# Optimization experiments

Hardware: AMD Instinct MI355X
Metric: run time of the kernel (lower is better)

Reference implementation:

```python
import jax, jax.numpy as jnp
import numpy as np
from jax import lax

D_MODEL = 1024
D_STATE = 16
D_CONV = 4
EXPAND = 2
D_INNER = EXPAND * D_MODEL          # 2048
DT_RANK = (D_MODEL + 15) // 16      # 64


def setup_inputs() -> dict:
    key = jax.random.key(0)
    ks = jax.random.split(key, 12)
    B, L = 2, 2048
    s = lambda *sh: 1.0 / np.sqrt(sh[-1])
    inp = {
        "x": jax.random.normal(ks[0], (B, L, D_MODEL), jnp.float32),
        "in_proj_w": jax.random.normal(ks[1], (2 * D_INNER, D_MODEL), jnp.float32) * s(0, D_MODEL),
        "conv_w": jax.random.normal(ks[2], (D_INNER, 1, D_CONV), jnp.float32) * s(0, D_CONV),
        "conv_b": jax.random.normal(ks[3], (D_INNER,), jnp.float32) * 0.01,
        "x_proj_w": jax.random.normal(ks[4], (DT_RANK + 2 * D_STATE, D_INNER), jnp.float32) * s(0, D_INNER),
        "dt_proj_w": jax.random.normal(ks[5], (D_INNER, DT_RANK), jnp.float32) * s(0, DT_RANK),
        "dt_proj_b": jax.random.normal(ks[6], (D_INNER,), jnp.float32) * 0.1 - 4.0,  # softplus(dt) small
        "A_log": jnp.log(jnp.broadcast_to(jnp.arange(1, D_STATE + 1, dtype=jnp.float32), (D_INNER, D_STATE))),
        "D": jnp.ones((D_INNER,), jnp.float32),
        "out_proj_w": jax.random.normal(ks[7], (D_MODEL, D_INNER), jnp.float32) * s(0, D_INNER),
        "ln_w": jnp.ones((D_MODEL,), jnp.float32),
        "ln_b": jnp.zeros((D_MODEL,), jnp.float32),
    }
    return inp


def _mamba(x, in_proj_w, conv_w, conv_b, x_proj_w, dt_proj_w, dt_proj_b, A_log, D, out_proj_w):
    B, L, _ = x.shape
    xz = jnp.einsum("bld,ed->ble", x, in_proj_w)          # [B,L,2*d_inner]
    xi, z = jnp.split(xz, 2, axis=-1)                       # each [B,L,d_inner]

    # causal depthwise conv1d over time
    xt = jnp.transpose(xi, (0, 2, 1))                       # [B,d_inner,L]
    xc = lax.conv_general_dilated(
        xt, conv_w, window_strides=(1,), padding=[(D_CONV - 1, 0)],
        dimension_numbers=("NCH", "OIH", "NCH"), feature_group_count=D_INNER)
    xc = jax.nn.silu(xc + conv_b[None, :, None])            # [B,d_inner,L]
    u = jnp.transpose(xc, (0, 2, 1))                        # [B,L,d_inner]

    x_dbl = jnp.einsum("bld,ed->ble", u, x_proj_w)          # [B,L,dt_rank+2N]
    dt, Bm, Cm = jnp.split(x_dbl, [DT_RANK, DT_RANK + D_STATE], axis=-1)
    delta = jax.nn.softplus(jnp.einsum("blr,dr->bld", dt, dt_proj_w) + dt_proj_b)  # [B,L,d_inner]

    A = -jnp.exp(A_log)                                     # [d_inner,N]

    def step(h, inputs):
        d_t, B_t, C_t, u_t = inputs                         # [B,d], [B,N], [B,N], [B,d]
        dA = jnp.exp(d_t[..., None] * A)                    # [B,d_inner,N]
        h = dA * h + (d_t * u_t)[..., None] * B_t[:, None, :]
        y_t = jnp.einsum("bdn,bn->bd", h, C_t)
        return h, y_t

    xs = (jnp.transpose(delta, (1, 0, 2)), jnp.transpose(Bm, (1, 0, 2)),
          jnp.transpose(Cm, (1, 0, 2)), jnp.transpose(u, (1, 0, 2)))
    h0 = jnp.zeros((B, D_INNER, D_STATE), x.dtype)
    _, ys = lax.scan(step, h0, xs)                          # ys [L,B,d_inner]
    y = jnp.transpose(ys, (1, 0, 2)) + u * D                # skip connection
    y = y * jax.nn.silu(z)                                  # gate
    return jnp.einsum("bld,ed->ble", y, out_proj_w)         # [B,L,d_model]


def reference(x, in_proj_w, conv_w, conv_b, x_proj_w, dt_proj_w, dt_proj_b,
              A_log, D, out_proj_w, ln_w, ln_b):
    residual = x
    y = _mamba(x, in_proj_w, conv_w, conv_b, x_proj_w, dt_proj_w, dt_proj_b,
               A_log, D, out_proj_w)
    # dropout is identity in eval; residual + LayerNorm
    h = y + residual
    mu = jnp.mean(h, axis=-1, keepdims=True)
    var = jnp.var(h, axis=-1, keepdims=True)
    return (h - mu) * lax.rsqrt(var + 1e-5) * ln_w + ln_b
```

## Files before the change

### kernel.cpp

```cpp
#include <hip/hip_runtime.h>

typedef unsigned short u16;
typedef __attribute__((ext_vector_type(8))) short bf8_t;
typedef __attribute__((ext_vector_type(4))) float f4_t;
typedef __attribute__((ext_vector_type(4))) unsigned short u16x4;
typedef __attribute__((ext_vector_type(8))) unsigned short u16x8;

__device__ __forceinline__ float b2f(u16 h) {
  union { unsigned u; float f; } v; v.u = ((unsigned)h) << 16; return v.f;
}
__device__ __forceinline__ u16 f2b(float f) {
  union { float f; unsigned u; } v; v.f = f;
  unsigned u = v.u;
  u += 0x7fffu + ((u >> 16) & 1u);
  return (u16)(u >> 16);
}

#define AS1C(p) ((const __attribute__((address_space(1))) void*)(p))
#define AS3(p)  ((__attribute__((address_space(3))) void*)(p))

__global__ __launch_bounds__(256)
void cvt_all(const float* __restrict__ x, const float* __restrict__ inW,
             const float* __restrict__ xprojW, const float* __restrict__ dtW,
             const float* __restrict__ outW,
             u16* __restrict__ xb, u16* __restrict__ inWb, u16* __restrict__ xpb,
             u16* __restrict__ dtWb, u16* __restrict__ outWb)
{
  int i = blockIdx.x * 256 + threadIdx.x;
  if (i >= 2703360) return;
  const float* s; u16* d; int off;
  if (i < 1048576)      { s = x;      d = xb;    off = i; }
  else if (i < 2097152) { s = inW;    d = inWb;  off = i - 1048576; }
  else if (i < 2146304) { s = xprojW; d = xpb;   off = i - 2097152; }
  else if (i < 2179072) { s = dtW;    d = dtWb;  off = i - 2146304; }
  else                  { s = outW;   d = outWb; off = i - 2179072; }
  f4_t v = *(const f4_t*)(s + (size_t)off * 4);
  u16x4 o;
#pragma unroll
  for (int j = 0; j < 4; ++j) o[j] = f2b(v[j]);
  *(u16x4*)(d + (size_t)off * 4) = o;
}

__device__ __forceinline__ void stage64(const u16* g, int ld, int row0, int rowmax,
                                        int k0, u16* lds, int wid, int lane) {
  int qg = (lane & 7) ^ ((lane >> 3) & 7);
#pragma unroll
  for (int c = 0; c < 4; ++c) {
    int chunk = wid * 4 + c;
    int r = row0 + chunk * 8 + (lane >> 3);
    if (r > rowmax) r = rowmax;
    const u16* gp = g + (size_t)r * ld + k0 + qg * 8;
    __builtin_amdgcn_global_load_lds(AS1C(gp), AS3(lds + chunk * 512), 16, 0, 0);
  }
}

template<int EPI>
__device__ __forceinline__ void gemm_body(const u16* __restrict__ A, int lda,
             const u16* __restrict__ Bt, int ldb,
             int Kblk, int Nact,
             u16* __restrict__ o16, float* __restrict__ of32,
             float* __restrict__ of32b, const float* __restrict__ biasf)
{
  __shared__ u16 lsA[128 * 64];
  __shared__ u16 lsB[128 * 64];
  const int tid = threadIdx.x;
  const int wid = tid >> 6, lane = tid & 63;
  const int wm = wid >> 1, wn = wid & 1;
  const int lrow = lane & 15;
  const int kq = lane >> 4;
  const int sw = lrow & 7;
  const int m0 = blockIdx.y * 128;
  const int n0 = (EPI == 1) ? 0 : blockIdx.x * 128;
  int kbase = 0;
  if (EPI == 1) kbase = blockIdx.x * Kblk;

  f4_t acc[4][4];
#pragma unroll
  for (int i = 0; i < 4; ++i)
#pragma unroll
    for (int j = 0; j < 4; ++j) acc[i][j] = {0.f, 0.f, 0.f, 0.f};

  for (int kt = kbase; kt < kbase + Kblk; kt += 64) {
    stage64(A,  lda, m0, 0x3fffffff, kt, lsA, wid, lane);
    stage64(Bt, ldb, n0, Nact - 1,   kt, lsB, wid, lane);
    __syncthreads();
#pragma unroll
    for (int h = 0; h < 2; ++h) {
      const int lk = ((h * 4 + kq) ^ sw) * 8;
      bf8_t af[4], bfr[4];
#pragma unroll
      for (int mi = 0; mi < 4; ++mi)
        af[mi] = *(const bf8_t*)&lsA[(wm * 64 + mi * 16 + lrow) * 64 + lk];
#pragma unroll
      for (int ni = 0; ni < 4; ++ni)
        bfr[ni] = *(const bf8_t*)&lsB[(wn * 64 + ni * 16 + lrow) * 64 + lk];
#pragma unroll
      for (int mi = 0; mi < 4; ++mi)
#pragma unroll
        for (int ni = 0; ni < 4; ++ni)
          acc[mi][ni] = __builtin_amdgcn_mfma_f32_16x16x32_bf16(af[mi], bfr[ni], acc[mi][ni], 0, 0, 0);
    }
    __syncthreads();
  }

  const int rq = (lane >> 4) * 4;
#pragma unroll
  for (int mi = 0; mi < 4; ++mi) {
#pragma unroll
    for (int ni = 0; ni < 4; ++ni) {
#pragma unroll
      for (int r = 0; r < 4; ++r) {
        int m = m0 + wm * 64 + mi * 16 + rq + r;
        int n = n0 + wn * 64 + ni * 16 + lrow;
        float v = acc[mi][ni][r];
        if (EPI == 1) {
          if (n < 96) of32[((size_t)blockIdx.x * 4096 + m) * 96 + n] = v;
        } else if (EPI == 2) {
          float t = v + biasf[n];
          float sp = (t > 20.f) ? t : log1pf(__expf(t));
          o16[(size_t)m * 2048 + n] = f2b(sp);
        }
      }
    }
  }
}

__global__ __launch_bounds__(256)
void gemm_xp(const u16* A, int lda, const u16* Bt, int ldb, int Kblk, int Nact,
             u16* o16, float* of32, float* of32b, const float* biasf)
{ gemm_body<1>(A, lda, Bt, ldb, Kblk, Nact, o16, of32, of32b, biasf); }

__global__ __launch_bounds__(256)
void gemm_dt(const u16* A, int lda, const u16* Bt, int ldb, int Kblk, int Nact,
             u16* o16, float* of32, float* of32b, const float* biasf)
{ gemm_body<2>(A, lda, Bt, ldb, Kblk, Nact, o16, of32, of32b, biasf); }


__device__ __forceinline__ void stageu(const u16* __restrict__ g, int ld,
                                       int row0, int k0, u16* ldsu,
                                       int wid, int lane) {
  int qg = (lane & 7) ^ ((lane >> 3) & 7);
#pragma unroll
  for (int j = 0; j < 2; ++j) {
    int rr = j * 64 + wid * 8 + (lane >> 3);
    const u16* gp = g + (size_t)(row0 + rr) * ld + k0 + qg * 8;
    __builtin_amdgcn_global_load_lds(AS1C(gp), AS3(ldsu + (j * 512 + wid * 64) * 8), 16, 0, 0);
  }
}

#define G8_BAR()   __builtin_amdgcn_s_barrier()
#define G8_LGKM0() do { asm volatile("s_waitcnt lgkmcnt(0)" ::: "memory"); \
                        __builtin_amdgcn_sched_barrier(0); } while (0)
#define G8_VM(N)   do { asm volatile("s_waitcnt vmcnt(" #N ")" ::: "memory"); \
                        __builtin_amdgcn_sched_barrier(0); } while (0)

#define RD_A(base, MH) do { \
  _Pragma("unroll") \
  for (int mi_ = 0; mi_ < 4; ++mi_) { \
    af[mi_][0] = *(const bf8_t*)((base) + arow + ((MH) * 64 + mi_ * 16) * 64 + aq0); \
    af[mi_][1] = *(const bf8_t*)((base) + arow + ((MH) * 64 + mi_ * 16) * 64 + aq1); \
  } } while (0)

#define RD_B(base, NH) do { \
  _Pragma("unroll") \
  for (int ni_ = 0; ni_ < 2; ++ni_) { \
    bfr[NH][ni_][0] = *(const bf8_t*)((base) + brow + ((NH) * 32 + ni_ * 16) * 64 + aq0); \
    bfr[NH][ni_][1] = *(const bf8_t*)((base) + brow + ((NH) * 32 + ni_ * 16) * 64 + aq1); \
  } } while (0)

#define MMA(MH, NH) do { \
  __builtin_amdgcn_s_setprio(1); \
  _Pragma("unroll") \
  for (int mi_ = 0; mi_ < 4; ++mi_) \
    _Pragma("unroll") \
    for (int ni_ = 0; ni_ < 2; ++ni_) { \
      acc[(MH) * 4 + mi_][(NH) * 2 + ni_] = __builtin_amdgcn_mfma_f32_16x16x32_bf16( \
          af[mi_][0], bfr[NH][ni_][0], acc[(MH) * 4 + mi_][(NH) * 2 + ni_], 0, 0, 0); \
      acc[(MH) * 4 + mi_][(NH) * 2 + ni_] = __builtin_amdgcn_mfma_f32_16x16x32_bf16( \
          af[mi_][1], bfr[NH][ni_][1], acc[(MH) * 4 + mi_][(NH) * 2 + ni_], 0, 0, 0); \
    } \
  __builtin_amdgcn_s_setprio(0); \
} while (0)

__global__ __launch_bounds__(512, 2)
void gemm8_in(const u16* __restrict__ A, const u16* __restrict__ Bt,
              u16* __restrict__ o16)
{
  __shared__ u16 ls[65536];
  const int tid = threadIdx.x;
  const int wid = tid >> 6, lane = tid & 63;
  const int wm = wid >> 2, wn = wid & 3;
  const int lrow = lane & 15;
  const int kq = lane >> 4;
  const int sw = lrow & 7;
  const int m0 = blockIdx.y * 256;
  const int n0 = blockIdx.x * 256;
  u16* lsA0 = ls;
  u16* lsB0 = ls + 16384;
  u16* lsA1 = ls + 32768;
  u16* lsB1 = ls + 49152;
  const int arow = (wm * 128 + lrow) * 64;
  const int brow = (wn * 64 + lrow) * 64;
  const int aq0 = (kq ^ sw) * 8;
  const int aq1 = ((4 + kq) ^ sw) * 8;

  f4_t acc[8][4];
#pragma unroll
  for (int i = 0; i < 8; ++i)
#pragma unroll
    for (int j = 0; j < 4; ++j) acc[i][j] = {0.f, 0.f, 0.f, 0.f};
  bf8_t af[4][2];
  bf8_t bfr[2][2][2];

  stageu(A,  1024, m0,        0, lsA0,        wid, lane);
  stageu(A,  1024, m0 + 128,  0, lsA0 + 8192, wid, lane);
  stageu(Bt, 1024, n0,        0, lsB0,        wid, lane);
  stageu(Bt, 1024, n0 + 128,  0, lsB0 + 8192, wid, lane);
  stageu(Bt, 1024, n0,       64, lsB1,        wid, lane);
  stageu(Bt, 1024, n0 + 128, 64, lsB1 + 8192, wid, lane);
  G8_VM(4); G8_BAR();

#pragma unroll 1
  for (int i = 0; i < 7; ++i) {
    const int ka1 = (2 * i + 1) * 64;
    const int k2  = ka1 + 64;
    const int kb3 = ka1 + 128;
    RD_A(lsA0, 0); RD_B(lsB0, 0); RD_B(lsB0, 1);
    stageu(A, 1024, m0,       ka1, lsA1,        wid, lane);
    stageu(A, 1024, m0 + 128, ka1, lsA1 + 8192, wid, lane);
    G8_BAR(); G8_LGKM0(); MMA(0, 0); MMA(0, 1); G8_BAR();
    RD_A(lsA0, 1);
    stageu(Bt, 1024, n0,       k2, lsB0,        wid, lane);
    stageu(Bt, 1024, n0 + 128, k2, lsB0 + 8192, wid, lane);
    G8_BAR(); G8_LGKM0(); MMA(1, 0); MMA(1, 1); G8_VM(4); G8_BAR();
    RD_A(lsA1, 0); RD_B(lsB1, 0); RD_B(lsB1, 1);
    stageu(A, 1024, m0,       k2, lsA0,        wid, lane);
    stageu(A, 1024, m0 + 128, k2, lsA0 + 8192, wid, lane);
    G8_BAR(); G8_LGKM0(); MMA(0, 0); MMA(0, 1); G8_BAR();
    RD_A(lsA1, 1);
    stageu(Bt, 1024, n0,       kb3, lsB1,        wid, lane);
    stageu(Bt, 1024, n0 + 128, kb3, lsB1 + 8192, wid, lane);
    G8_BAR(); G8_LGKM0(); MMA(1, 0); MMA(1, 1); G8_VM(4); G8_BAR();
  }

  {
    const int ka1 = 960;
    RD_A(lsA0, 0); RD_B(lsB0, 0); RD_B(lsB0, 1);
    stageu(A, 1024, m0,       ka1, lsA1,        wid, lane);
    stageu(A, 1024, m0 + 128, ka1, lsA1 + 8192, wid, lane);
    G8_BAR(); G8_LGKM0(); MMA(0, 0); MMA(0, 1); G8_BAR();
    RD_A(lsA0, 1);
    G8_BAR(); G8_LGKM0(); MMA(1, 0); MMA(1, 1); G8_VM(0); G8_BAR();
    RD_A(lsA1, 0); RD_B(lsB1, 0); RD_B(lsB1, 1);
    G8_BAR(); G8_LGKM0(); MMA(0, 0); MMA(0, 1); G8_BAR();
    RD_A(lsA1, 1);
    G8_LGKM0(); MMA(1, 0); MMA(1, 1);
  }

  const int rq = (lane >> 4) * 4;
#pragma unroll
  for (int mi = 0; mi < 8; ++mi) {
#pragma unroll
    for (int ni = 0; ni < 4; ++ni) {
#pragma unroll
      for (int r = 0; r < 4; ++r) {
        int m = m0 + wm * 128 + mi * 16 + rq + r;
        int n = n0 + wn * 64 + ni * 16 + lrow;
        float v = acc[mi][ni][r];
        if (n < 2048) o16[(size_t)m * 2048 + n] = f2b(v);
        else          o16[(size_t)8388608 + (size_t)m * 2048 + (n - 2048)] = f2b(v);
      }
    }
  }
}


#define ORD_A(base, MH) do { \
  _Pragma("unroll") \
  for (int mi_ = 0; mi_ < 2; ++mi_) { \
    af[mi_][0] = *(const bf8_t*)((base) + arow + ((MH) * 32 + mi_ * 16) * 64 + aq0); \
    af[mi_][1] = *(const bf8_t*)((base) + arow + ((MH) * 32 + mi_ * 16) * 64 + aq1); \
  } } while (0)

#define OMMA(MH, NH) do { \
  __builtin_amdgcn_s_setprio(1); \
  _Pragma("unroll") \
  for (int mi_ = 0; mi_ < 2; ++mi_) \
    _Pragma("unroll") \
    for (int ni_ = 0; ni_ < 2; ++ni_) { \
      acc[(MH) * 2 + mi_][(NH) * 2 + ni_] = __builtin_amdgcn_mfma_f32_16x16x32_bf16( \
          af[mi_][0], bfr[NH][ni_][0], acc[(MH) * 2 + mi_][(NH) * 2 + ni_], 0, 0, 0); \
      acc[(MH) * 2 + mi_][(NH) * 2 + ni_] = __builtin_amdgcn_mfma_f32_16x16x32_bf16( \
          af[mi_][1], bfr[NH][ni_][1], acc[(MH) * 2 + mi_][(NH) * 2 + ni_], 0, 0, 0); \
    } \
  __builtin_amdgcn_s_setprio(0); \
} while (0)

__global__ __launch_bounds__(512, 2)
void gemm8_out(const u16* __restrict__ A, const u16* __restrict__ Bt,
               float* __restrict__ of32, float* __restrict__ of32b)
{
  __shared__ u16 ls[49152];
  const int tid = threadIdx.x;
  const int wid = tid >> 6, lane = tid & 63;
  const int wm = wid >> 2, wn = wid & 3;
  const int lrow = lane & 15;
  const int kq = lane >> 4;
  const int sw = lrow & 7;
  const int m0 = blockIdx.y * 128;
  const int n0 = blockIdx.x * 256;
  const int kbase = blockIdx.z * 1024;
  u16* lsA0 = ls;
  u16* lsB0 = ls + 8192;
  u16* lsA1 = ls + 24576;
  u16* lsB1 = ls + 32768;
  const int arow = (wm * 64 + lrow) * 64;
  const int brow = (wn >> 1) * 8192 + ((wn & 1) * 64 + lrow) * 64;
  const int aq0 = (kq ^ sw) * 8;
  const int aq1 = ((4 + kq) ^ sw) * 8;

  f4_t acc[4][4];
#pragma unroll
  for (int i = 0; i < 4; ++i)
#pragma unroll
    for (int j = 0; j < 4; ++j) acc[i][j] = {0.f, 0.f, 0.f, 0.f};
  bf8_t af[2][2];
  bf8_t bfr[2][2][2];

  stageu(A,  2048, m0,        kbase,      lsA0,        wid, lane);
  stageu(Bt, 2048, n0,        kbase,      lsB0,        wid, lane);
  stageu(Bt, 2048, n0 + 128,  kbase,      lsB0 + 8192, wid, lane);
  stageu(Bt, 2048, n0,        kbase + 64, lsB1,        wid, lane);
  stageu(Bt, 2048, n0 + 128,  kbase + 64, lsB1 + 8192, wid, lane);
  G8_VM(4); G8_BAR();

#pragma unroll 1
  for (int i = 0; i < 7; ++i) {
    const int k1 = kbase + (2 * i + 1) * 64, k2 = k1 + 64, k3 = k1 + 128;
    ORD_A(lsA0, 0); RD_B(lsB0, 0);
    stageu(A, 2048, m0, k1, lsA1, wid, lane);
    G8_BAR(); G8_LGKM0(); OMMA(0, 0); G8_BAR();
    RD_B(lsB0, 1);
    G8_BAR(); G8_LGKM0(); OMMA(0, 1); G8_BAR();
    ORD_A(lsA0, 1);
    stageu(Bt, 2048, n0, k2, lsB0, wid, lane);
    G8_BAR(); G8_LGKM0(); OMMA(1, 0); G8_BAR();
    stageu(Bt, 2048, n0 + 128, k2, lsB0 + 8192, wid, lane);
    G8_BAR(); G8_LGKM0(); OMMA(1, 1); G8_VM(4); G8_BAR();
    ORD_A(lsA1, 0); RD_B(lsB1, 0);
    stageu(A, 2048, m0, k2, lsA0, wid, lane);
    G8_BAR(); G8_LGKM0(); OMMA(0, 0); G8_BAR();
    RD_B(lsB1, 1);
    G8_BAR(); G8_LGKM0(); OMMA(0, 1); G8_BAR();
    ORD_A(lsA1, 1);
    stageu(Bt, 2048, n0, k3, lsB1, wid, lane);
    G8_BAR(); G8_LGKM0(); OMMA(1, 0); G8_BAR();
    stageu(Bt, 2048, n0 + 128, k3, lsB1 + 8192, wid, lane);
    G8_BAR(); G8_LGKM0(); OMMA(1, 1); G8_VM(4); G8_BAR();
  }

  {
    const int k1 = kbase + 960;
    ORD_A(lsA0, 0); RD_B(lsB0, 0);
    stageu(A, 2048, m0, k1, lsA1, wid, lane);
    G8_BAR(); G8_LGKM0(); OMMA(0, 0); G8_BAR();
    RD_B(lsB0, 1);
    G8_BAR(); G8_LGKM0(); OMMA(0, 1); G8_BAR();
    ORD_A(lsA0, 1);
    G8_BAR(); G8_LGKM0(); OMMA(1, 0); G8_BAR();
    G8_BAR(); G8_LGKM0(); OMMA(1, 1); G8_VM(0); G8_BAR();
    ORD_A(lsA1, 0); RD_B(lsB1, 0);
    G8_BAR(); G8_LGKM0(); OMMA(0, 0); G8_BAR();
    RD_B(lsB1, 1);
    G8_BAR(); G8_LGKM0(); OMMA(0, 1); G8_BAR();
    ORD_A(lsA1, 1);
    G8_BAR(); G8_LGKM0(); OMMA(1, 0); G8_BAR();
    G8_LGKM0(); OMMA(1, 1);
  }

  float* dst = blockIdx.z ? of32b : of32;
  const int rq = (lane >> 4) * 4;
#pragma unroll
  for (int mi = 0; mi < 4; ++mi) {
#pragma unroll
    for (int ni = 0; ni < 4; ++ni) {
#pragma unroll
      for (int r = 0; r < 4; ++r) {
        int m = m0 + wm * 64 + mi * 16 + rq + r;
        int n = n0 + wn * 64 + ni * 16 + lrow;
        dst[(size_t)m * 1024 + n] = acc[mi][ni][r];
      }
    }
  }
}

__global__ __launch_bounds__(256)
void xproj_reduce(const float* __restrict__ part, u16* __restrict__ dtA,
                  float* __restrict__ bc)
{
  int idx = blockIdx.x * 256 + threadIdx.x;
  int m = idx / 96, n = idx - m * 96;
  float s = 0.f;
#pragma unroll
  for (int p = 0; p < 8; ++p) s += part[(size_t)p * 393216 + idx];
  if (n < 64) dtA[(size_t)m * 64 + n] = f2b(s);
  else        bc[(size_t)m * 32 + (n - 64)] = s;
}

__global__ __launch_bounds__(256)
void conv_silu(const u16* __restrict__ xib, const float* __restrict__ cw,
               const float* __restrict__ cb, u16* __restrict__ ub)
{
  int i = blockIdx.x * 256 + threadIdx.x;
  int c8 = (i & 255) * 8;
  int row = i >> 8;
  int l = row & 2047;
  const u16* base = xib + (size_t)row * 2048 + c8;
  u16x8 x0 = {0,0,0,0,0,0,0,0}, x1 = x0, x2 = x0, x3;
  x3 = *(const u16x8*)(base);
  if (l >= 1) x2 = *(const u16x8*)(base - 2048);
  if (l >= 2) x1 = *(const u16x8*)(base - 2 * 2048);
  if (l >= 3) x0 = *(const u16x8*)(base - 3 * 2048);
  f4_t cb0 = *(const f4_t*)(cb + c8);
  f4_t cb1 = *(const f4_t*)(cb + c8 + 4);
  u16x8 o;
#pragma unroll
  for (int j = 0; j < 8; ++j) {
    f4_t w = *(const f4_t*)(cw + (size_t)(c8 + j) * 4);
    float a = (j < 4 ? cb0[j] : cb1[j - 4])
            + w[0] * b2f(x0[j]) + w[1] * b2f(x1[j])
            + w[2] * b2f(x2[j]) + w[3] * b2f(x3[j]);
    float s = a / (1.f + __expf(-a));
    o[j] = f2b(s);
  }
  *(u16x8*)(ub + (size_t)row * 2048 + c8) = o;
}

__global__ __launch_bounds__(256)
void scan_s1(const u16* __restrict__ delta_bf, const u16* __restrict__ ub,
             const float* __restrict__ bc, const float* __restrict__ alog,
             u16* __restrict__ S, float* __restrict__ Q)
{
  int blk = blockIdx.x;
  int g = blk & 7, c = (blk >> 3) & 31, b = blk >> 8;
  int d = g * 256 + threadIdx.x;
  float Av[16];
#pragma unroll
  for (int nq = 0; nq < 4; ++nq) {
    f4_t al = *(const f4_t*)(alog + (size_t)d * 16 + nq * 4);
#pragma unroll
    for (int j = 0; j < 4; ++j) Av[nq * 4 + j] = -__expf(al[j]);
  }
  float Av0 = Av[0];
  bool st = true;
#pragma unroll
  for (int n = 1; n < 16; ++n)
    st = st && (fabsf(Av[n] - (float)(n + 1) * Av0) <= 1e-3f * (float)(n + 1));
  f4_t Qr[4];
#pragma unroll
  for (int nq = 0; nq < 4; ++nq) Qr[nq] = {0.f,0.f,0.f,0.f};
  float Sd = 0.f;
  int row0 = b * 2048 + c * 64;
  if (st) {
#pragma unroll 2
    for (int i = 0; i < 64; ++i) {
      size_t row = (size_t)(row0 + i);
      float dlt = b2f(delta_bf[row * 2048 + d]);
      float uv  = b2f(ub[row * 2048 + d]);
      const float* bp = bc + row * 32;
      f4_t Bv[4];
#pragma unroll
      for (int nq = 0; nq < 4; ++nq) Bv[nq] = *(const f4_t*)(bp + nq * 4);
      float du = dlt * uv;
      float e1 = __expf(dlt * Av0);
      float a = e1;
      Sd += dlt;
#pragma unroll
      for (int n = 0; n < 16; ++n) {
        Qr[n >> 2][n & 3] = a * Qr[n >> 2][n & 3] + du * Bv[n >> 2][n & 3];
        a *= e1;
      }
    }
  } else {
#pragma unroll 2
    for (int i = 0; i < 64; ++i) {
      size_t row = (size_t)(row0 + i);
      float dlt = b2f(delta_bf[row * 2048 + d]);
      float uv  = b2f(ub[row * 2048 + d]);
      const float* bp = bc + row * 32;
      f4_t Bv[4];
#pragma unroll
      for (int nq = 0; nq < 4; ++nq) Bv[nq] = *(const f4_t*)(bp + nq * 4);
      float du = dlt * uv;
      Sd += dlt;
#pragma unroll
      for (int n = 0; n < 16; ++n) {
        float a = __expf(dlt * Av[n]);
        Qr[n >> 2][n & 3] = a * Qr[n >> 2][n & 3] + du * Bv[n >> 2][n & 3];
      }
    }
  }
  S[(size_t)(b * 32 + c) * 2048 + d] = f2b(Sd);
  size_t o = ((size_t)((b * 32 + c) * 2048 + d)) * 16;
#pragma unroll
  for (int nq = 0; nq < 4; ++nq)
    *(f4_t*)(Q + o + nq * 4) = Qr[nq];
}

__global__ __launch_bounds__(256)
void scan_comb(const u16* __restrict__ S16, float* __restrict__ Q,
               const float* __restrict__ alog)
{
  int idx = blockIdx.x * 256 + threadIdx.x;
  int b = idx >> 15, dn = idx & 32767;
  int d = dn >> 4;
  float Av = -__expf(alog[dn]);
  size_t qbase = (size_t)b * 1048576 + dn;
  size_t sbase = (size_t)b * 65536 + d;
  float H = 0.f;
#pragma unroll
  for (int cg = 0; cg < 2; ++cg) {
    float sv[16], qv[16];
#pragma unroll
    for (int j = 0; j < 16; ++j) {
      int c = cg * 16 + j;
      qv[j] = Q[qbase + (size_t)c * 32768];
      sv[j] = b2f(S16[sbase + (size_t)c * 2048]);
    }
#pragma unroll
    for (int j = 0; j < 16; ++j) {
      int c = cg * 16 + j;
      Q[qbase + (size_t)c * 32768] = H;
      H = __expf(Av * sv[j]) * H + qv[j];
    }
  }
}

__global__ __launch_bounds__(256)
void scan_s3(const u16* __restrict__ delta_bf, const u16* __restrict__ ub,
             const float* __restrict__ bc, const float* __restrict__ alog,
             const float* __restrict__ Q, const float* __restrict__ Dw,
             u16* __restrict__ zy)
{
  int blk = blockIdx.x;
  int g = blk & 7, c = (blk >> 3) & 31, b = blk >> 8;
  int d = g * 256 + threadIdx.x;
  float Av[16];
#pragma unroll
  for (int nq = 0; nq < 4; ++nq) {
    f4_t al = *(const f4_t*)(alog + (size_t)d * 16 + nq * 4);
#pragma unroll
    for (int j = 0; j < 4; ++j) Av[nq * 4 + j] = -__expf(al[j]);
  }
  float Av0 = Av[0];
  bool st = true;
#pragma unroll
  for (int n = 1; n < 16; ++n)
    st = st && (fabsf(Av[n] - (float)(n + 1) * Av0) <= 1e-3f * (float)(n + 1));
  f4_t h4[4];
  size_t o = ((size_t)((b * 32 + c) * 2048 + d)) * 16;
#pragma unroll
  for (int nq = 0; nq < 4; ++nq) h4[nq] = *(const f4_t*)(Q + o + nq * 4);
  float Dv = Dw[d];
  int row0 = b * 2048 + c * 64;
  if (st) {
#pragma unroll 2
    for (int i = 0; i < 64; ++i) {
      size_t row = (size_t)(row0 + i);
      float dlt = b2f(delta_bf[row * 2048 + d]);
      float uv  = b2f(ub[row * 2048 + d]);
      const float* bp = bc + row * 32;
      f4_t Bv[4], Cv[4];
#pragma unroll
      for (int nq = 0; nq < 4; ++nq) { Bv[nq] = *(const f4_t*)(bp + nq * 4); Cv[nq] = *(const f4_t*)(bp + 16 + nq * 4); }
      float du = dlt * uv;
      float e1 = __expf(dlt * Av0);
      float a = e1;
      float y = 0.f;
#pragma unroll
      for (int n = 0; n < 16; ++n) {
        float hn = a * h4[n >> 2][n & 3] + du * Bv[n >> 2][n & 3];
        h4[n >> 2][n & 3] = hn;
        y += hn * Cv[n >> 2][n & 3];
        a *= e1;
      }
      float zv = b2f(zy[row * 2048 + d]);
      float ov = (y + Dv * uv) * (zv / (1.f + __expf(-zv)));
      zy[row * 2048 + d] = f2b(ov);
    }
  } else {
#pragma unroll 2
    for (int i = 0; i < 64; ++i) {
      size_t row = (size_t)(row0 + i);
      float dlt = b2f(delta_bf[row * 2048 + d]);
      float uv  = b2f(ub[row * 2048 + d]);
      const float* bp = bc + row * 32;
      f4_t Bv[4], Cv[4];
#pragma unroll
      for (int nq = 0; nq < 4; ++nq) { Bv[nq] = *(const f4_t*)(bp + nq * 4); Cv[nq] = *(const f4_t*)(bp + 16 + nq * 4); }
      float du = dlt * uv;
      float y = 0.f;
#pragma unroll
      for (int n = 0; n < 16; ++n) {
        float a = __expf(dlt * Av[n]);
        float hn = a * h4[n >> 2][n & 3] + du * Bv[n >> 2][n & 3];
        h4[n >> 2][n & 3] = hn;
        y += hn * Cv[n >> 2][n & 3];
      }
      float zv = b2f(zy[row * 2048 + d]);
      float ov = (y + Dv * uv) * (zv / (1.f + __expf(-zv)));
      zy[row * 2048 + d] = f2b(ov);
    }
  }
}

__global__ __launch_bounds__(256)
void ln_kernel(const float* __restrict__ hp0, const float* __restrict__ hp1,
               const float* __restrict__ xin,
               const float* __restrict__ lnw, const float* __restrict__ lnb,
               float* __restrict__ outp)
{
  __shared__ float ssum[4], ssq[4];
  int row = blockIdx.x, t = threadIdx.x;
  f4_t h0 = *(const f4_t*)(hp0 + (size_t)row * 1024 + t * 4);
  f4_t h1 = *(const f4_t*)(hp1 + (size_t)row * 1024 + t * 4);
  f4_t xv = *(const f4_t*)(xin + (size_t)row * 1024 + t * 4);
  float v[4], s = 0.f, q = 0.f;
#pragma unroll
  for (int j = 0; j < 4; ++j) { v[j] = h0[j] + h1[j] + xv[j]; s += v[j]; q += v[j] * v[j]; }
#pragma unroll
  for (int m = 32; m; m >>= 1) { s += __shfl_xor(s, m, 64); q += __shfl_xor(q, m, 64); }
  int wv = t >> 6;
  if ((t & 63) == 0) { ssum[wv] = s; ssq[wv] = q; }
  __syncthreads();
  s = ssum[0] + ssum[1] + ssum[2] + ssum[3];
  q = ssq[0] + ssq[1] + ssq[2] + ssq[3];
  float mu = s * (1.f / 1024.f);
  float var = q * (1.f / 1024.f) - mu * mu;
  float rs = rsqrtf(var + 1e-5f);
  f4_t o;
#pragma unroll
  for (int j = 0; j < 4; ++j)
    o[j] = (v[j] - mu) * rs * lnw[t * 4 + j] + lnb[t * 4 + j];
  *(f4_t*)(outp + (size_t)row * 1024 + t * 4) = o;
}

extern "C" void kernel_launch(void* const* d_in, const int* in_sizes, int n_in,
                              void* d_out, int out_size, void* d_ws, size_t ws_size,
                              hipStream_t stream)
{
  const float* x      = (const float*)d_in[0];
  const float* inW    = (const float*)d_in[1];
  const float* convW  = (const float*)d_in[2];
  const float* convB  = (const float*)d_in[3];
  const float* xprojW = (const float*)d_in[4];
  const float* dtW    = (const float*)d_in[5];
  const float* dtB    = (const float*)d_in[6];
  const float* alog   = (const float*)d_in[7];
  const float* Dw     = (const float*)d_in[8];
  const float* outW   = (const float*)d_in[9];
  const float* lnw    = (const float*)d_in[10];
  const float* lnb    = (const float*)d_in[11];
  float* out = (float*)d_out;

  char* ws = (char*)d_ws;
  u16*   xiz    = (u16*)(ws);
  u16*   zy     = xiz + 8388608;
  u16*   xb     = (u16*)(ws + 33554432);
  u16*   inWb   = xb + 4194304;
  u16*   u_bf   = (u16*)(ws + 33554432);
  u16*   dtA    = (u16*)(ws + 50331648);
  float* bc     = (float*)(ws + 50855936);
  u16*   xprojWb= (u16*)(ws + 51380224);
  u16*   dtWb   = (u16*)(ws + 51773440);
  u16*   outWb  = (u16*)(ws + 52035584);
  u16*   delta  = xiz;
  float* hpart1 = (float*)(ws);
  float* hpart0 = (float*)d_out;
  float* xpart  = (float*)d_out;
  u16*   Sbuf   = dtA;
  float* Qbuf   = (float*)d_out;

  dim3 blk(256);
  cvt_all<<<10560, blk, 0, stream>>>(x, inW, xprojW, dtW, outW,
                                     xb, inWb, xprojWb, dtWb, outWb);
  gemm8_in<<<dim3(16, 16), dim3(512), 0, stream>>>(xb, inWb, xiz);
  conv_silu<<<4096, blk, 0, stream>>>(xiz, convW, convB, u_bf);
  gemm_xp<<<dim3(8, 32), blk, 0, stream>>>(u_bf, 2048, xprojWb, 2048, 256, 96, nullptr, xpart, nullptr, nullptr);
  xproj_reduce<<<1536, blk, 0, stream>>>(xpart, dtA, bc);
  gemm_dt<<<dim3(16, 32), blk, 0, stream>>>(dtA, 64, dtWb, 64, 64, 2048, delta, nullptr, nullptr, dtB);
  scan_s1<<<512, blk, 0, stream>>>(delta, u_bf, bc, alog, Sbuf, Qbuf);
  scan_comb<<<256, blk, 0, stream>>>(Sbuf, Qbuf, alog);
  scan_s3<<<512, blk, 0, stream>>>(delta, u_bf, bc, alog, Qbuf, Dw, zy);
  gemm8_out<<<dim3(4, 32, 2), dim3(512), 0, stream>>>(zy, outWb, hpart0, hpart1);
  ln_kernel<<<4096, blk, 0, stream>>>(hpart0, hpart1, x, lnw, lnb, out);
}
```

Baseline: 316.7 us.

## Preload second A half, remap tiles per XCD, and halve scan chunk length

In the input-projection GEMM, both halves of the A fragments are now read from LDS up front. A partial lgkmcnt wait lets the first MFMA batch start while the second half is still arriving, which also removes one barrier per half-step. The tile index is remapped so neighbouring tiles land on the same XCD for better L2 reuse. The chunked scan now uses 64 chunks of 32 steps instead of 32 of 64, doubling the grid for more parallelism at the cost of a longer combine pass and larger S/Q buffers. Extra fragment registers may raise VGPR pressure, and the bigger Q buffer must still fit in the reused output buffer.

```diff
diff --git a/kernel.cpp b/kernel.cpp
--- a/kernel.cpp
+++ b/kernel.cpp
@@ -149,7 +149,10 @@
 }
 
 #define G8_BAR()   __builtin_amdgcn_s_barrier()
+#define G8_SB()    __builtin_amdgcn_sched_barrier(0)
 #define G8_LGKM0() do { asm volatile("s_waitcnt lgkmcnt(0)" ::: "memory"); \
+                        __builtin_amdgcn_sched_barrier(0); } while (0)
+#define G8_LGKM8() do { asm volatile("s_waitcnt lgkmcnt(8)" ::: "memory"); \
                         __builtin_amdgcn_sched_barrier(0); } while (0)
 #define G8_VM(N)   do { asm volatile("s_waitcnt vmcnt(" #N ")" ::: "memory"); \
                         __builtin_amdgcn_sched_barrier(0); } while (0)
@@ -159,6 +162,13 @@
   for (int mi_ = 0; mi_ < 4; ++mi_) { \
     af[mi_][0] = *(const bf8_t*)((base) + arow + ((MH) * 64 + mi_ * 16) * 64 + aq0); \
     af[mi_][1] = *(const bf8_t*)((base) + arow + ((MH) * 64 + mi_ * 16) * 64 + aq1); \
+  } } while (0)
+
+#define RD_A2(base) do { \
+  _Pragma("unroll") \
+  for (int mi_ = 0; mi_ < 4; ++mi_) { \
+    af2[mi_][0] = *(const bf8_t*)((base) + arow + (64 + mi_ * 16) * 64 + aq0); \
+    af2[mi_][1] = *(const bf8_t*)((base) + arow + (64 + mi_ * 16) * 64 + aq1); \
   } } while (0)
 
 #define RD_B(base, NH) do { \
@@ -182,6 +192,20 @@
   __builtin_amdgcn_s_setprio(0); \
 } while (0)
 
+#define MMA2(NH) do { \
+  __builtin_amdgcn_s_setprio(1); \
+  _Pragma("unroll") \
+  for (int mi_ = 0; mi_ < 4; ++mi_) \
+    _Pragma("unroll") \
+    for (int ni_ = 0; ni_ < 2; ++ni_) { \
+      acc[4 + mi_][(NH) * 2 + ni_] = __builtin_amdgcn_mfma_f32_16x16x32_bf16( \
+          af2[mi_][0], bfr[NH][ni_][0], acc[4 + mi_][(NH) * 2 + ni_], 0, 0, 0); \
+      acc[4 + mi_][(NH) * 2 + ni_] = __builtin_amdgcn_mfma_f32_16x16x32_bf16( \
+          af2[mi_][1], bfr[NH][ni_][1], acc[4 + mi_][(NH) * 2 + ni_], 0, 0, 0); \
+    } \
+  __builtin_amdgcn_s_setprio(0); \
+} while (0)
+
 __global__ __launch_bounds__(512, 2)
 void gemm8_in(const u16* __restrict__ A, const u16* __restrict__ Bt,
               u16* __restrict__ o16)
@@ -193,8 +217,10 @@
   const int lrow = lane & 15;
   const int kq = lane >> 4;
   const int sw = lrow & 7;
-  const int m0 = blockIdx.y * 256;
-  const int n0 = blockIdx.x * 256;
+  const int id  = blockIdx.y * 16 + blockIdx.x;
+  const int xcd = id & 7, idx = id >> 3;
+  const int m0 = ((xcd >> 1) * 4 + (idx >> 3)) * 256;
+  const int n0 = ((xcd & 1) * 8 + (idx & 7)) * 256;
   u16* lsA0 = ls;
   u16* lsB0 = ls + 16384;
   u16* lsA1 = ls + 32768;
@@ -210,6 +236,7 @@
 #pragma unroll
     for (int j = 0; j < 4; ++j) acc[i][j] = {0.f, 0.f, 0.f, 0.f};
   bf8_t af[4][2];
+  bf8_t af2[4][2];
   bf8_t bfr[2][2][2];
 
   stageu(A,  1024, m0,        0, lsA0,        wid, lane);
@@ -226,35 +253,39 @@
     const int k2  = ka1 + 64;
     const int kb3 = ka1 + 128;
     RD_A(lsA0, 0); RD_B(lsB0, 0); RD_B(lsB0, 1);
+    G8_SB();
+    RD_A2(lsA0);
     stageu(A, 1024, m0,       ka1, lsA1,        wid, lane);
     stageu(A, 1024, m0 + 128, ka1, lsA1 + 8192, wid, lane);
-    G8_BAR(); G8_LGKM0(); MMA(0, 0); MMA(0, 1); G8_BAR();
-    RD_A(lsA0, 1);
+    G8_BAR(); G8_LGKM8(); MMA(0, 0); MMA(0, 1); G8_BAR();
     stageu(Bt, 1024, n0,       k2, lsB0,        wid, lane);
     stageu(Bt, 1024, n0 + 128, k2, lsB0 + 8192, wid, lane);
-    G8_BAR(); G8_LGKM0(); MMA(1, 0); MMA(1, 1); G8_VM(4); G8_BAR();
+    G8_LGKM0(); MMA2(0); MMA2(1); G8_VM(4); G8_BAR();
     RD_A(lsA1, 0); RD_B(lsB1, 0); RD_B(lsB1, 1);
+    G8_SB();
+    RD_A2(lsA1);
     stageu(A, 1024, m0,       k2, lsA0,        wid, lane);
     stageu(A, 1024, m0 + 128, k2, lsA0 + 8192, wid, lane);
-    G8_BAR(); G8_LGKM0(); MMA(0, 0); MMA(0, 1); G8_BAR();
-    RD_A(lsA1, 1);
+    G8_BAR(); G8_LGKM8(); MMA(0, 0); MMA(0, 1); G8_BAR();
     stageu(Bt, 1024, n0,       kb3, lsB1,        wid, lane);
     stageu(Bt, 1024, n0 + 128, kb3, lsB1 + 8192, wid, lane);
-    G8_BAR(); G8_LGKM0(); MMA(1, 0); MMA(1, 1); G8_VM(4); G8_BAR();
+    G8_LGKM0(); MMA2(0); MMA2(1); G8_VM(4); G8_BAR();
   }
 
   {
     const int ka1 = 960;
     RD_A(lsA0, 0); RD_B(lsB0, 0); RD_B(lsB0, 1);
+    G8_SB();
+    RD_A2(lsA0);
     stageu(A, 1024, m0,       ka1, lsA1,        wid, lane);
     stageu(A, 1024, m0 + 128, ka1, lsA1 + 8192, wid, lane);
-    G8_BAR(); G8_LGKM0(); MMA(0, 0); MMA(0, 1); G8_BAR();
-    RD_A(lsA0, 1);
-    G8_BAR(); G8_LGKM0(); MMA(1, 0); MMA(1, 1); G8_VM(0); G8_BAR();
+    G8_BAR(); G8_LGKM8(); MMA(0, 0); MMA(0, 1); G8_BAR();
+    G8_LGKM0(); MMA2(0); MMA2(1); G8_VM(0); G8_BAR();
     RD_A(lsA1, 0); RD_B(lsB1, 0); RD_B(lsB1, 1);
-    G8_BAR(); G8_LGKM0(); MMA(0, 0); MMA(0, 1); G8_BAR();
-    RD_A(lsA1, 1);
-    G8_LGKM0(); MMA(1, 0); MMA(1, 1);
+    G8_SB();
+    RD_A2(lsA1);
+    G8_BAR(); G8_LGKM8(); MMA(0, 0); MMA(0, 1); G8_BAR();
+    G8_LGKM0(); MMA2(0); MMA2(1);
   }
 
   const int rq = (lane >> 4) * 4;
@@ -442,7 +473,7 @@
              u16* __restrict__ S, float* __restrict__ Q)
 {
   int blk = blockIdx.x;
-  int g = blk & 7, c = (blk >> 3) & 31, b = blk >> 8;
+  int g = blk & 7, c = (blk >> 3) & 63, b = blk >> 9;
   int d = g * 256 + threadIdx.x;
   float Av[16];
 #pragma unroll
@@ -460,10 +491,10 @@
 #pragma unroll
   for (int nq = 0; nq < 4; ++nq) Qr[nq] = {0.f,0.f,0.f,0.f};
   float Sd = 0.f;
-  int row0 = b * 2048 + c * 64;
+  int row0 = b * 2048 + c * 32;
   if (st) {
 #pragma unroll 2
-    for (int i = 0; i < 64; ++i) {
+    for (int i = 0; i < 32; ++i) {
       size_t row = (size_t)(row0 + i);
       float dlt = b2f(delta_bf[row * 2048 + d]);
       float uv  = b2f(ub[row * 2048 + d]);
@@ -483,7 +514,7 @@
     }
   } else {
 #pragma unroll 2
-    for (int i = 0; i < 64; ++i) {
+    for (int i = 0; i < 32; ++i) {
       size_t row = (size_t)(row0 + i);
       float dlt = b2f(delta_bf[row * 2048 + d]);
       float uv  = b2f(ub[row * 2048 + d]);
@@ -500,8 +531,8 @@
       }
     }
   }
-  S[(size_t)(b * 32 + c) * 2048 + d] = f2b(Sd);
-  size_t o = ((size_t)((b * 32 + c) * 2048 + d)) * 16;
+  S[(size_t)(b * 64 + c) * 2048 + d] = f2b(Sd);
+  size_t o = ((size_t)((b * 64 + c) * 2048 + d)) * 16;
 #pragma unroll
   for (int nq = 0; nq < 4; ++nq)
     *(f4_t*)(Q + o + nq * 4) = Qr[nq];
@@ -515,11 +546,11 @@
   int b = idx >> 15, dn = idx & 32767;
   int d = dn >> 4;
   float Av = -__expf(alog[dn]);
-  size_t qbase = (size_t)b * 1048576 + dn;
-  size_t sbase = (size_t)b * 65536 + d;
+  size_t qbase = (size_t)b * 2097152 + dn;
+  size_t sbase = (size_t)b * 131072 + d;
   float H = 0.f;
 #pragma unroll
-  for (int cg = 0; cg < 2; ++cg) {
+  for (int cg = 0; cg < 4; ++cg) {
     float sv[16], qv[16];
 #pragma unroll
     for (int j = 0; j < 16; ++j) {
@@ -543,7 +574,7 @@
              u16* __restrict__ zy)
 {
   int blk = blockIdx.x;
-  int g = blk & 7, c = (blk >> 3) & 31, b = blk >> 8;
+  int g = blk & 7, c = (blk >> 3) & 63, b = blk >> 9;
   int d = g * 256 + threadIdx.x;
   float Av[16];
 #pragma unroll
@@ -558,14 +589,14 @@
   for (int n = 1; n < 16; ++n)
     st = st && (fabsf(Av[n] - (float)(n + 1) * Av0) <= 1e-3f * (float)(n + 1));
   f4_t h4[4];
-  size_t o = ((size_t)((b * 32 + c) * 2048 + d)) * 16;
+  size_t o = ((size_t)((b * 64 + c) * 2048 + d)) * 16;
 #pragma unroll
   for (int nq = 0; nq < 4; ++nq) h4[nq] = *(const f4_t*)(Q + o + nq * 4);
   float Dv = Dw[d];
-  int row0 = b * 2048 + c * 64;
+  int row0 = b * 2048 + c * 32;
   if (st) {
 #pragma unroll 2
-    for (int i = 0; i < 64; ++i) {
+    for (int i = 0; i < 32; ++i) {
       size_t row = (size_t)(row0 + i);
       float dlt = b2f(delta_bf[row * 2048 + d]);
       float uv  = b2f(ub[row * 2048 + d]);
@@ -590,7 +621,7 @@
     }
   } else {
 #pragma unroll 2
-    for (int i = 0; i < 64; ++i) {
+    for (int i = 0; i < 32; ++i) {
       size_t row = (size_t)(row0 + i);
       float dlt = b2f(delta_bf[row * 2048 + d]);
       float uv  = b2f(ub[row * 2048 + d]);
@@ -689,9 +720,9 @@
   gemm_xp<<<dim3(8, 32), blk, 0, stream>>>(u_bf, 2048, xprojWb, 2048, 256, 96, nullptr, xpart, nullptr, nullptr);
   xproj_reduce<<<1536, blk, 0, stream>>>(xpart, dtA, bc);
   gemm_dt<<<dim3(16, 32), blk, 0, stream>>>(dtA, 64, dtWb, 64, 64, 2048, delta, nullptr, nullptr, dtB);
-  scan_s1<<<512, blk, 0, stream>>>(delta, u_bf, bc, alog, Sbuf, Qbuf);
+  scan_s1<<<1024, blk, 0, stream>>>(delta, u_bf, bc, alog, Sbuf, Qbuf);
   scan_comb<<<256, blk, 0, stream>>>(Sbuf, Qbuf, alog);
-  scan_s3<<<512, blk, 0, stream>>>(delta, u_bf, bc, alog, Qbuf, Dw, zy);
+  scan_s3<<<1024, blk, 0, stream>>>(delta, u_bf, bc, alog, Qbuf, Dw, zy);
   gemm8_out<<<dim3(4, 32, 2), dim3(512), 0, stream>>>(zy, outWb, hpart0, hpart1);
   ln_kernel<<<4096, blk, 0, stream>>>(hpart0, hpart1, x, lnw, lnb, out);
 }
```

Measured after the change: 316.6 us. Within noise of the previous version (-0.0%).
